# Optimization experiments

Measured on AMD Instinct MI355X. Metric: run time of the kernel, lower is better.

## Reference

```python
import jax, jax.numpy as jnp
import numpy as np

NUM_CLASSES = 3
EPS = 1e-6
POS_IOU = 0.5   # assumed thresholds of utils.match_anchors_to_targets
NEG_IOU = 0.4
NEG_RATIO = 3


def _make_anchors(H, W, stride):
    sizes = np.array([3.0, 4.0, 5.0]) * stride  # 3 anchors per location
    ys = (np.arange(H) + 0.5) * stride
    xs = (np.arange(W) + 0.5) * stride
    cy, cx = np.meshgrid(ys, xs, indexing='ij')
    cx = cx[:, :, None]
    cy = cy[:, :, None]
    s = sizes[None, None, :]
    boxes = np.stack([cx - s / 2, cy - s / 2, cx + s / 2, cy + s / 2], axis=-1)  # [H,W,A,4]
    return boxes.reshape(-1, 4).astype(np.float32)


def setup_inputs() -> dict:
    key = jax.random.key(0)
    B, G, A, C = 64, 32, 3, NUM_CLASSES
    scales = [(128, 128, 8), (64, 64, 16), (32, 32, 32)]
    ks = jax.random.split(key, 6)
    inp = {}
    for i, (H, W, s) in enumerate(scales):
        inp[f'pred{i}'] = jax.random.normal(ks[i], (B, A * (5 + C), H, W), jnp.float32)
        inp[f'anchors{i}'] = jnp.asarray(_make_anchors(H, W, s))
    c = jax.random.uniform(ks[3], (B, G, 2), minval=100.0, maxval=900.0)
    wh = jax.random.uniform(ks[4], (B, G, 2), minval=16.0, maxval=200.0)
    inp['gt_boxes'] = jnp.concatenate([c - wh / 2, c + wh / 2], axis=-1)
    inp['gt_labels'] = jax.random.randint(ks[5], (B, G), 0, C)
    return inp


def _smooth_l1(x):
    ax = jnp.abs(x)
    return jnp.where(ax < 1.0, 0.5 * x * x, ax - 0.5)


def _bce_logits(x, t):
    return jnp.maximum(x, 0.0) - x * t + jnp.log1p(jnp.exp(-jnp.abs(x)))


def _pairwise_iou(a, b):  # a [N,4], b [G,4] -> [N,G]
    lt = jnp.maximum(a[:, None, :2], b[None, :, :2])
    rb = jnp.minimum(a[:, None, 2:], b[None, :, 2:])
    wh = jnp.clip(rb - lt, 0.0)
    inter = wh[..., 0] * wh[..., 1]
    area_a = (a[:, 2] - a[:, 0]) * (a[:, 3] - a[:, 1])
    area_b = (b[:, 2] - b[:, 0]) * (b[:, 3] - b[:, 1])
    return inter / (area_a[:, None] + area_b[None, :] - inter + 1e-9)


def _per_image(p, anc, gtb, gtl):
    # p: [N, 5+C], anc: [N,4], gtb: [G,4], gtl: [G]
    iou = _pairwise_iou(anc, gtb)
    best_iou = jnp.max(iou, axis=1)
    best_idx = jnp.argmax(iou, axis=1)
    m_boxes = gtb[best_idx]
    m_labels = gtl[best_idx]
    pos = best_iou >= POS_IOU
    neg = best_iou < NEG_IOU
    posf = pos.astype(p.dtype)

    ax = (anc[:, 0] + anc[:, 2]) * 0.5
    ay = (anc[:, 1] + anc[:, 3]) * 0.5
    aw = jnp.maximum(anc[:, 2] - anc[:, 0], EPS)
    ah = jnp.maximum(anc[:, 3] - anc[:, 1], EPS)
    gx = (m_boxes[:, 0] + m_boxes[:, 2]) * 0.5
    gy = (m_boxes[:, 1] + m_boxes[:, 3]) * 0.5
    gw = jnp.maximum(m_boxes[:, 2] - m_boxes[:, 0], EPS)
    gh = jnp.maximum(m_boxes[:, 3] - m_boxes[:, 1], EPS)
    t_tx = (gx - ax) / aw
    t_ty = (gy - ay) / ah
    t_tw = jnp.log(gw / aw)
    t_th = jnp.log(gh / ah)

    loc = (posf * (_smooth_l1(p[:, 0] - t_tx) + _smooth_l1(p[:, 1] - t_ty)
                   + _smooth_l1(p[:, 2] - t_tw) + _smooth_l1(p[:, 3] - t_th))).sum()

    obj_all = _bce_logits(p[:, 4], posf)
    # hard negative mining on detached loss: top (3*max(1,num_pos)) negatives
    num_pos = pos.sum()
    num_keep = NEG_RATIO * jnp.maximum(1, num_pos)
    neg_loss = jnp.where(neg, jax.lax.stop_gradient(obj_all), -1e9)
    order = jnp.argsort(-neg_loss)
    N = order.shape[0]
    ranks = jnp.zeros((N,), dtype=jnp.int32).at[order].set(jnp.arange(N, dtype=jnp.int32))
    selected = neg & (ranks < num_keep)
    obj = (obj_all * (posf + selected.astype(p.dtype))).sum()

    logp = jax.nn.log_softmax(p[:, 5:], axis=-1)
    tgt = jnp.maximum(m_labels, 0)
    ce = -jnp.take_along_axis(logp, tgt[:, None], axis=1)[:, 0]
    cls = (posf * ce).sum()
    return loc, obj, cls


def reference(pred0, pred1, pred2, anchors0, anchors1, anchors2, gt_boxes, gt_labels):
    B = pred0.shape[0]
    C = NUM_CLASSES
    total = jnp.float32(0.0)
    for pred, anc in ((pred0, anchors0), (pred1, anchors1), (pred2, anchors2)):
        N = anc.shape[0]
        p = pred.transpose(0, 2, 3, 1).reshape(B, N, 5 + C)  # [B, H*W*A, 5+C]
        loc, obj, cls = jax.vmap(lambda pb, gb, gl, a=anc: _per_image(pb, a, gb, gl))(
            p, gt_boxes, gt_labels)
        total = total + loc.sum() + obj.sum() + cls.sum()
    return total / jnp.maximum(1.0, float(B))
```

## Files before the change

### kernel.cpp

```cpp
#include <hip/hip_runtime.h>
#include <math.h>

#define BLK 256
#define SBLK 1024
#define NBINS 2048
#define CSH 42
#define QMASK ((1ULL << CSH) - 1ULL)

__device__ __forceinline__ float bce_logits(float x, float t){
    return fmaxf(x, 0.f) - x * t + log1pf(expf(-fabsf(x)));
}
__device__ __forceinline__ float smooth_l1(float x){
    float ax = fabsf(x);
    return ax < 1.f ? 0.5f * x * x : ax - 0.5f;
}

__global__ __launch_bounds__(BLK)
void det_map_all(const float* __restrict__ pred0,
                 const float* __restrict__ pred1,
                 const float* __restrict__ pred2,
                 const float* __restrict__ gtb,
                 const int*   __restrict__ gtl,
                 float* __restrict__ vals,
                 float* __restrict__ loss_slot,
                 int*   __restrict__ pcnt_slot,
                 unsigned* __restrict__ done_cnt,
                 int B)
{
    const int b  = blockIdx.y;
    const int bx = blockIdx.x;

    const float* pred; int s, qloc, P, logW; float stride_f; size_t vbase;
    if (bx < 48){      s=0; pred=pred0; P=16384; logW=7; stride_f= 8.f; qloc= bx      << 8; vbase=(size_t)b*49152; }
    else if (bx < 60){ s=1; pred=pred1; P= 4096; logW=6; stride_f=16.f; qloc=(bx-48) << 8; vbase=(size_t)B*49152 + (size_t)b*12288; }
    else {             s=2; pred=pred2; P= 1024; logW=5; stride_f=32.f; qloc=(bx-60) << 8; vbase=(size_t)B*49152 + (size_t)B*12288 + (size_t)b*3072; }

    const int tid = threadIdx.x;
    const int lq  = 2*logW - 2;
    const int Q4  = 1 << lq;
    const int a   = qloc >> lq;
    const int q   = qloc - a*Q4 + tid;
    const int pix0 = q << 2;

    const float half = 0.5f * (float)(3 + a) * stride_f;

    const int pixLo = (qloc - a*Q4) << 2;
    const int y0 = pixLo >> logW, y1 = (pixLo + BLK*4 - 1) >> logW;
    const float ymin = ((float)y0 + 0.5f) * stride_f - half;
    const float ymax = ((float)y1 + 0.5f) * stride_f + half;

    __shared__ float4 sg[32];
    __shared__ float  sarea[32];
    __shared__ int    sl[32];
    __shared__ int    s_cnt;

    {
        bool keep = false; float4 G;
        if (tid < 32){
            G = ((const float4*)gtb)[b * 32 + tid];
            keep = (G.y < ymax) && (G.w > ymin);
        }
        unsigned long long m = __ballot(keep);
        if (tid < 64){
            if (keep){
                int idx = (int)__popcll(m & ((1ULL << tid) - 1ULL));
                sg[idx] = G;
                sarea[idx] = (G.z - G.x) * (G.w - G.y);
                sl[idx] = gtl[b * 32 + tid];
            }
            if (tid == 0) s_cnt = (int)__popcll(m);
        }
    }
    __syncthreads();
    const int cnt = s_cnt;

    const int x0 = pix0 & ((1 << logW) - 1);
    const int y  = pix0 >> logW;
    const float cy = ((float)y + 0.5f) * stride_f;
    const float Ay = cy - half, Ay2 = cy + half;
    const float sz = 2.f * half;
    const float area_a = sz * sz;

    float ax[4], az[4];
    #pragma unroll
    for (int j = 0; j < 4; ++j){
        float cx = ((float)(x0 + j) + 0.5f) * stride_f;
        ax[j] = cx - half; az[j] = cx + half;
    }

    float bi[4] = {-1.f, -1.f, -1.f, -1.f};
    float bd[4] = { 1.f,  1.f,  1.f,  1.f};
    int   bg[4] = {0, 0, 0, 0};

    for (int g = 0; g < cnt; ++g){
        const float4 G = sg[g];
        const float sab = area_a + sarea[g];
        const float h = fmaxf(fminf(Ay2, G.w) - fmaxf(Ay, G.y), 0.f);
        #pragma unroll
        for (int j = 0; j < 4; ++j){
            float wdt = fmaxf(fminf(az[j], G.z) - fmaxf(ax[j], G.x), 0.f);
            float inter = wdt * h;
            float d = (sab - inter) + 1e-9f;
            if (inter * bd[j] > bi[j] * d){ bi[j] = inter; bd[j] = d; bg[j] = g; }
        }
    }

    const size_t cP = (size_t)P;
    const float* pp = pred + ((size_t)b * 24 + (size_t)a * 8) * cP + (size_t)pix0;
    const float4 p4v = *(const float4*)(pp + 4 * cP);
    const float p4a[4] = {p4v.x, p4v.y, p4v.z, p4v.w};

    float vout[4];
    float loss = 0.f; int pc = 0;
    #pragma unroll
    for (int j = 0; j < 4; ++j){
        const bool pos = 2.f * bi[j] >= bd[j];
        const bool neg = bi[j] < 0.4f * bd[j];
        vout[j] = neg ? bce_logits(p4a[j], 0.f) : -1.f;
        if (pos){
            pc++;
            const float4 G = sg[bg[j]];
            float axc = (ax[j] + az[j]) * 0.5f, ayc = (Ay + Ay2) * 0.5f;
            float aw = fmaxf(az[j] - ax[j], 1e-6f), ah = fmaxf(Ay2 - Ay, 1e-6f);
            float gxc = (G.x + G.z) * 0.5f, gyc = (G.y + G.w) * 0.5f;
            float gw = fmaxf(G.z - G.x, 1e-6f), gh = fmaxf(G.w - G.y, 1e-6f);
            float p0 = pp[0 * cP + j];
            float p1 = pp[1 * cP + j];
            float p2 = pp[2 * cP + j];
            float p3 = pp[3 * cP + j];
            loss += smooth_l1(p0 - (gxc - axc) / aw);
            loss += smooth_l1(p1 - (gyc - ayc) / ah);
            loss += smooth_l1(p2 - logf(gw / aw));
            loss += smooth_l1(p3 - logf(gh / ah));
            loss += bce_logits(p4a[j], 1.f);
            float c0 = pp[5 * cP + j];
            float c1 = pp[6 * cP + j];
            float c2 = pp[7 * cP + j];
            float m = fmaxf(c0, fmaxf(c1, c2));
            float lse = m + logf(expf(c0 - m) + expf(c1 - m) + expf(c2 - m));
            int tg = sl[bg[j]];
            float ct = (tg == 0) ? c0 : ((tg == 1) ? c1 : c2);
            loss += lse - ct;
        }
    }
    float4 vo = {vout[0], vout[1], vout[2], vout[3]};
    *(float4*)(vals + vbase + ((size_t)(qloc - a*Q4 + tid + a*Q4)) * 4) = vo;

    for (int off = 32; off > 0; off >>= 1){
        loss += __shfl_down(loss, off);
        pc   += __shfl_down(pc, off);
    }
    __shared__ float wsum[BLK / 64];
    __shared__ int   wcnt[BLK / 64];
    if ((tid & 63) == 0){ wsum[tid >> 6] = loss; wcnt[tid >> 6] = pc; }
    __syncthreads();
    if (tid == 0){
        float S = 0.f; int C = 0;
        for (int i = 0; i < BLK / 64; ++i){ S += wsum[i]; C += wcnt[i]; }
        loss_slot[b * 63 + bx] = S;
        pcnt_slot[b * 63 + bx] = C;
        if (b == 0 && bx == 0) *done_cnt = 0u;
    }
}

__global__ __launch_bounds__(SBLK)
void det_select(const float* __restrict__ vals,
                const float* __restrict__ loss_slot,
                const int* __restrict__ pcnt_slot,
                double* __restrict__ slice_tot,
                unsigned* __restrict__ done_cnt,
                float* __restrict__ out, int B)
{
    const int sb = blockIdx.x;
    const int s = sb / B, b = sb - s * B;
    const int N = (s == 0) ? 49152 : (s == 1) ? 12288 : 3072;
    size_t base = 0;
    if (s >= 1) base += (size_t)B * 49152;
    if (s >= 2) base += (size_t)B * 12288;
    const float* V = vals + base + (size_t)b * (size_t)N;

    const int tid = threadIdx.x;
    const int lane = tid & 63, w = tid >> 6;
    const int rep = w & 1;

    __shared__ unsigned long long h[2][NBINS];
    __shared__ unsigned long long waveT[16];
    __shared__ unsigned long long waveOff[17];
    __shared__ unsigned long long sh_aboveQ;
    __shared__ double sh_sel;
    __shared__ float sh_ml;
    __shared__ int sh_b1, sh_rem, sh_done, sh_K, sh_last;

    {
        const int nb   = (s == 0) ? 48 : (s == 1) ? 12 : 3;
        const int off0 = b * 63 + ((s == 0) ? 0 : (s == 1) ? 48 : 60);
        float ml = 0.f; int C = 0;
        if (tid < nb){ ml = loss_slot[off0 + tid]; C = pcnt_slot[off0 + tid]; }
        if (tid < 64){
            for (int off = 32; off > 0; off >>= 1){
                ml += __shfl_down(ml, off);
                C  += __shfl_down(C, off);
            }
            if (tid == 0){
                sh_ml = ml; sh_K = 3 * max(1, C);
                sh_rem = sh_K; sh_done = 0;
            }
        }
    }

    for (int round = 0; round < 2; ++round){
        for (int i = tid; i < NBINS; i += SBLK){ h[0][i] = 0ULL; h[1][i] = 0ULL; }
        __syncthreads();
        const int b1 = sh_b1;

        if (round == 0 || !sh_done){
            for (int i = tid * 4; i < N; i += SBLK * 4){
                float4 v4 = *(const float4*)(V + i);
                #pragma unroll
                for (int j = 0; j < 4; ++j){
                    float v = (j == 0) ? v4.x : (j == 1) ? v4.y : (j == 2) ? v4.z : v4.w;
                    if (!(v >= 0.f)) continue;
                    float t = v * 256.f;
                    int bin0 = min((int)t, NBINS - 1);
                    int key;
                    if (round == 0) key = bin0;
                    else {
                        if (bin0 != b1) continue;
                        float frac = t - (float)bin0;
                        key = min((int)(frac * 2048.f), NBINS - 1);
                    }
                    unsigned long long p = (1ULL << CSH) |
                        (unsigned long long)(unsigned)(int)(v * 4194304.f);
                    atomicAdd(&h[rep][key], p);
                }
            }
        }
        __syncthreads();
        if (sh_done) break;

        const int bhi = NBINS - 1 - 2 * tid;
        const unsigned long long c0p = h[0][bhi] + h[1][bhi];
        const unsigned long long c1p = h[0][bhi - 1] + h[1][bhi - 1];
        const unsigned long long pair = c0p + c1p;
        unsigned long long ci = pair;
        #pragma unroll
        for (int off = 1; off < 64; off <<= 1){
            unsigned long long cu = __shfl_up(ci, off);
            if (lane >= off) ci += cu;
        }
        if (lane == 63) waveT[w] = ci;
        __syncthreads();
        if (tid == 0){
            unsigned long long acc = 0ULL;
            #pragma unroll
            for (int i = 0; i < 16; ++i){ waveOff[i] = acc; acc += waveT[i]; }
            waveOff[16] = acc;
            if (round == 0 && sh_K >= (int)(acc >> CSH)){
                sh_done = 1;
                sh_sel = (double)(acc & QMASK) * (1.0 / 4194304.0);
            }
        }
        __syncthreads();
        if (sh_done) break;

        const int rem = sh_rem;
        const unsigned long long giP = waveOff[w] + ci;
        const unsigned long long geP = giP - pair;
        const int gi = (int)(giP >> CSH);
        const int ge = (int)(geP >> CSH);
        if (ge < rem && rem <= gi){
            const int c0 = (int)(c0p >> CSH);
            int bin, aboveC; unsigned long long aboveQ;
            if (ge + c0 >= rem){ bin = bhi;     aboveC = ge;      aboveQ = geP & QMASK; }
            else               { bin = bhi - 1; aboveC = ge + c0; aboveQ = (geP + c0p) & QMASK; }
            const int newRem = rem - aboveC;
            if (round == 0){
                sh_b1 = bin; sh_rem = newRem; sh_aboveQ = aboveQ;
            } else {
                float thresh = (float)sh_b1 * (1.f / 256.f) + (float)bin * (1.f / 524288.f);
                sh_sel = (double)(sh_aboveQ + aboveQ) * (1.0 / 4194304.0)
                       + (double)newRem * (double)thresh;
            }
        }
        __syncthreads();
    }

    if (tid == 0){
        slice_tot[sb] = (double)sh_ml + sh_sel;
        __threadfence();
        unsigned t = atomicAdd(done_cnt, 1u);
        sh_last = (t == (unsigned)(gridDim.x - 1));
        if (sh_last) __threadfence();
    }
    __syncthreads();
    if (sh_last){
        double p = (tid < 3 * B) ? slice_tot[tid] : 0.0;
        for (int off = 32; off > 0; off >>= 1) p += __shfl_down(p, off);
        __shared__ double wred[16];
        if (lane == 0) wred[w] = p;
        __syncthreads();
        if (tid == 0){
            double tot = 0.0;
            for (int i = 0; i < 16; ++i) tot += wred[i];
            out[0] = (float)(tot / (double)B);
        }
    }
}

extern "C" void kernel_launch(void* const* d_in, const int* in_sizes, int n_in,
                              void* d_out, int out_size, void* d_ws, size_t ws_size,
                              hipStream_t stream)
{
    const float* gtb = (const float*)d_in[6];
    const int*   gtl = (const int*)d_in[7];
    const int B = in_sizes[6] / (32 * 4);

    unsigned* done      = (unsigned*)d_ws;
    double*   slice_tot = (double*)((char*)d_ws + 64);
    float*    loss_slot = (float*)((char*)d_ws + 2048);
    int*      pcnt_slot = (int*)((char*)d_ws + 2048 + 16384);
    float*    vals      = (float*)((char*)d_ws + 36864);

    det_map_all<<<dim3(63, B), BLK, 0, stream>>>(
        (const float*)d_in[0], (const float*)d_in[2], (const float*)d_in[4],
        gtb, gtl, vals, loss_slot, pcnt_slot, done, B);
    det_select<<<dim3(3 * B), SBLK, 0, stream>>>(
        vals, loss_slot, pcnt_slot, slice_tot, done, (float*)d_out, B);
}
```

Measured before the change: 208.9 us.

## Fuse hard-negative selection into map kernel via last-block-per-slice ticket

Merges the separate selection kernel into the per-anchor map kernel. The last block to finish each (scale, image) slice, detected with an atomic ticket counter, runs the two-level histogram top-K selection. The first-level histogram shrinks to 1024 bins and the second level to 2048 sub-bins, both sized for 256-thread blocks, and a memset clears the counters before launch. This removes one kernel launch and the gap between the two kernels, and lets selection overlap with map work from other slices. In exchange, selection now runs on 256 threads instead of 1024, which may lengthen the tail for the large scale-0 slices.

```diff
diff --git a/kernel.cpp b/kernel.cpp
--- a/kernel.cpp
+++ b/kernel.cpp
@@ -2,8 +2,8 @@
 #include <math.h>
 
 #define BLK 256
-#define SBLK 1024
-#define NBINS 2048
+#define NB1 1024
+#define NB2 2048
 #define CSH 42
 #define QMASK ((1ULL << CSH) - 1ULL)
 
@@ -16,31 +16,35 @@
 }
 
 __global__ __launch_bounds__(BLK)
-void det_map_all(const float* __restrict__ pred0,
-                 const float* __restrict__ pred1,
-                 const float* __restrict__ pred2,
-                 const float* __restrict__ gtb,
-                 const int*   __restrict__ gtl,
-                 float* __restrict__ vals,
-                 float* __restrict__ loss_slot,
-                 int*   __restrict__ pcnt_slot,
-                 unsigned* __restrict__ done_cnt,
-                 int B)
+void det_all(const float* __restrict__ pred0,
+             const float* __restrict__ pred1,
+             const float* __restrict__ pred2,
+             const float* __restrict__ gtb,
+             const int*   __restrict__ gtl,
+             float* __restrict__ vals,
+             float* __restrict__ loss_slot,
+             int*   __restrict__ pcnt_slot,
+             unsigned* __restrict__ slice_tk,
+             double* __restrict__ slice_tot,
+             unsigned* __restrict__ done_tk,
+             float* __restrict__ out, int B)
 {
     const int b  = blockIdx.y;
     const int bx = blockIdx.x;
 
-    const float* pred; int s, qloc, P, logW; float stride_f; size_t vbase;
-    if (bx < 48){      s=0; pred=pred0; P=16384; logW=7; stride_f= 8.f; qloc= bx      << 8; vbase=(size_t)b*49152; }
-    else if (bx < 60){ s=1; pred=pred1; P= 4096; logW=6; stride_f=16.f; qloc=(bx-48) << 8; vbase=(size_t)B*49152 + (size_t)b*12288; }
-    else {             s=2; pred=pred2; P= 1024; logW=5; stride_f=32.f; qloc=(bx-60) << 8; vbase=(size_t)B*49152 + (size_t)B*12288 + (size_t)b*3072; }
-
+    const float* pred; int s, qloc, P, logW, nb; float stride_f; size_t vbase;
+    if (bx < 48){      s=0; pred=pred0; P=16384; logW=7; nb=48; stride_f= 8.f; qloc= bx      << 8; vbase=(size_t)b*49152; }
+    else if (bx < 60){ s=1; pred=pred1; P= 4096; logW=6; nb=12; stride_f=16.f; qloc=(bx-48) << 8; vbase=(size_t)B*49152 + (size_t)b*12288; }
+    else {             s=2; pred=pred2; P= 1024; logW=5; nb= 3; stride_f=32.f; qloc=(bx-60) << 8; vbase=(size_t)B*49152 + (size_t)B*12288 + (size_t)b*3072; }
+
+    const int sb  = s * B + b;
     const int tid = threadIdx.x;
+    const int lane = tid & 63, w = tid >> 6;
+
     const int lq  = 2*logW - 2;
     const int Q4  = 1 << lq;
     const int a   = qloc >> lq;
-    const int q   = qloc - a*Q4 + tid;
-    const int pix0 = q << 2;
+    const int pix0 = (qloc - a*Q4 + tid) << 2;
 
     const float half = 0.5f * (float)(3 + a) * stride_f;
 
@@ -53,6 +57,15 @@
     __shared__ float  sarea[32];
     __shared__ int    sl[32];
     __shared__ int    s_cnt;
+    __shared__ unsigned long long hsel[2][NB1];
+    __shared__ unsigned long long waveT[4];
+    __shared__ unsigned long long waveOff[5];
+    __shared__ unsigned long long sh_aboveQ;
+    __shared__ double sh_sel;
+    __shared__ float  sh_ml;
+    __shared__ float  wsum[4];
+    __shared__ int    wcnt[4];
+    __shared__ int    sh_b1, sh_rem, sh_done, sh_K, sh_win, sh_last;
 
     {
         bool keep = false; float4 G;
@@ -78,8 +91,7 @@
     const int y  = pix0 >> logW;
     const float cy = ((float)y + 0.5f) * stride_f;
     const float Ay = cy - half, Ay2 = cy + half;
-    const float sz = 2.f * half;
-    const float area_a = sz * sz;
+    const float area_a = (2.f * half) * (2.f * half);
 
     float ax[4], az[4];
     #pragma unroll
@@ -144,55 +156,34 @@
         }
     }
     float4 vo = {vout[0], vout[1], vout[2], vout[3]};
-    *(float4*)(vals + vbase + ((size_t)(qloc - a*Q4 + tid + a*Q4)) * 4) = vo;
+    *(float4*)(vals + vbase + (size_t)(qloc - a*Q4 + tid + a*Q4) * 4) = vo;
 
     for (int off = 32; off > 0; off >>= 1){
         loss += __shfl_down(loss, off);
         pc   += __shfl_down(pc, off);
     }
-    __shared__ float wsum[BLK / 64];
-    __shared__ int   wcnt[BLK / 64];
-    if ((tid & 63) == 0){ wsum[tid >> 6] = loss; wcnt[tid >> 6] = pc; }
+    if (lane == 0){ wsum[w] = loss; wcnt[w] = pc; }
     __syncthreads();
     if (tid == 0){
         float S = 0.f; int C = 0;
-        for (int i = 0; i < BLK / 64; ++i){ S += wsum[i]; C += wcnt[i]; }
+        for (int i = 0; i < 4; ++i){ S += wsum[i]; C += wcnt[i]; }
         loss_slot[b * 63 + bx] = S;
         pcnt_slot[b * 63 + bx] = C;
-        if (b == 0 && bx == 0) *done_cnt = 0u;
-    }
-}
-
-__global__ __launch_bounds__(SBLK)
-void det_select(const float* __restrict__ vals,
-                const float* __restrict__ loss_slot,
-                const int* __restrict__ pcnt_slot,
-                double* __restrict__ slice_tot,
-                unsigned* __restrict__ done_cnt,
-                float* __restrict__ out, int B)
-{
-    const int sb = blockIdx.x;
-    const int s = sb / B, b = sb - s * B;
+        __threadfence();
+        unsigned old = atomicAdd(&slice_tk[sb], 1u);
+        sh_win = (old == (unsigned)(nb - 1));
+        if (sh_win) __threadfence();
+    }
+    __syncthreads();
+    if (!sh_win) return;
+
     const int N = (s == 0) ? 49152 : (s == 1) ? 12288 : 3072;
     size_t base = 0;
     if (s >= 1) base += (size_t)B * 49152;
     if (s >= 2) base += (size_t)B * 12288;
     const float* V = vals + base + (size_t)b * (size_t)N;
 
-    const int tid = threadIdx.x;
-    const int lane = tid & 63, w = tid >> 6;
-    const int rep = w & 1;
-
-    __shared__ unsigned long long h[2][NBINS];
-    __shared__ unsigned long long waveT[16];
-    __shared__ unsigned long long waveOff[17];
-    __shared__ unsigned long long sh_aboveQ;
-    __shared__ double sh_sel;
-    __shared__ float sh_ml;
-    __shared__ int sh_b1, sh_rem, sh_done, sh_K, sh_last;
-
     {
-        const int nb   = (s == 0) ? 48 : (s == 1) ? 12 : 3;
         const int off0 = b * 63 + ((s == 0) ? 0 : (s == 1) ? 48 : 60);
         float ml = 0.f; int C = 0;
         if (tid < nb){ ml = loss_slot[off0 + tid]; C = pcnt_slot[off0 + tid]; }
@@ -201,48 +192,33 @@
                 ml += __shfl_down(ml, off);
                 C  += __shfl_down(C, off);
             }
-            if (tid == 0){
-                sh_ml = ml; sh_K = 3 * max(1, C);
-                sh_rem = sh_K; sh_done = 0;
-            }
-        }
-    }
-
-    for (int round = 0; round < 2; ++round){
-        for (int i = tid; i < NBINS; i += SBLK){ h[0][i] = 0ULL; h[1][i] = 0ULL; }
-        __syncthreads();
-        const int b1 = sh_b1;
-
-        if (round == 0 || !sh_done){
-            for (int i = tid * 4; i < N; i += SBLK * 4){
-                float4 v4 = *(const float4*)(V + i);
-                #pragma unroll
-                for (int j = 0; j < 4; ++j){
-                    float v = (j == 0) ? v4.x : (j == 1) ? v4.y : (j == 2) ? v4.z : v4.w;
-                    if (!(v >= 0.f)) continue;
-                    float t = v * 256.f;
-                    int bin0 = min((int)t, NBINS - 1);
-                    int key;
-                    if (round == 0) key = bin0;
-                    else {
-                        if (bin0 != b1) continue;
-                        float frac = t - (float)bin0;
-                        key = min((int)(frac * 2048.f), NBINS - 1);
-                    }
-                    unsigned long long p = (1ULL << CSH) |
-                        (unsigned long long)(unsigned)(int)(v * 4194304.f);
-                    atomicAdd(&h[rep][key], p);
-                }
-            }
-        }
-        __syncthreads();
-        if (sh_done) break;
-
-        const int bhi = NBINS - 1 - 2 * tid;
-        const unsigned long long c0p = h[0][bhi] + h[1][bhi];
-        const unsigned long long c1p = h[0][bhi - 1] + h[1][bhi - 1];
-        const unsigned long long pair = c0p + c1p;
-        unsigned long long ci = pair;
+            if (tid == 0){ sh_ml = ml; sh_K = 3 * max(1, C); sh_done = 0; }
+        }
+    }
+    for (int i = tid; i < NB1; i += BLK){ hsel[0][i] = 0ULL; hsel[1][i] = 0ULL; }
+    __syncthreads();
+
+    const int rep = w & 1;
+    for (int i = tid * 4; i < N; i += BLK * 4){
+        float4 v4 = *(const float4*)(V + i);
+        #pragma unroll
+        for (int j = 0; j < 4; ++j){
+            float v = (j == 0) ? v4.x : (j == 1) ? v4.y : (j == 2) ? v4.z : v4.w;
+            if (!(v >= 0.f)) continue;
+            int bin = min((int)(v * 128.f), NB1 - 1);
+            unsigned long long p = (1ULL << CSH) |
+                (unsigned long long)(unsigned)(int)(v * 4194304.f);
+            atomicAdd(&hsel[rep][bin], p);
+        }
+    }
+    __syncthreads();
+
+    {
+        const int start = NB1 - 4 * (tid + 1);
+        unsigned long long chunk[4]; unsigned long long tot = 0ULL;
+        #pragma unroll
+        for (int i = 0; i < 4; ++i){ chunk[i] = hsel[0][start+i] + hsel[1][start+i]; tot += chunk[i]; }
+        unsigned long long ci = tot;
         #pragma unroll
         for (int off = 1; off < 64; off <<= 1){
             unsigned long long cu = __shfl_up(ci, off);
@@ -253,34 +229,99 @@
         if (tid == 0){
             unsigned long long acc = 0ULL;
             #pragma unroll
-            for (int i = 0; i < 16; ++i){ waveOff[i] = acc; acc += waveT[i]; }
-            waveOff[16] = acc;
-            if (round == 0 && sh_K >= (int)(acc >> CSH)){
+            for (int i = 0; i < 4; ++i){ waveOff[i] = acc; acc += waveT[i]; }
+            waveOff[4] = acc;
+            if (sh_K >= (int)(acc >> CSH)){
                 sh_done = 1;
                 sh_sel = (double)(acc & QMASK) * (1.0 / 4194304.0);
             }
         }
         __syncthreads();
-        if (sh_done) break;
-
+        if (!sh_done){
+            const int K = sh_K;
+            const unsigned long long giP = waveOff[w] + ci;
+            const unsigned long long geP = giP - tot;
+            const int gi = (int)(giP >> CSH);
+            const int ge = (int)(geP >> CSH);
+            if (ge < K && K <= gi){
+                int aboveC = ge;
+                unsigned long long aboveQ = geP & QMASK;
+                #pragma unroll
+                for (int i = 3; i >= 0; --i){
+                    int c = (int)(chunk[i] >> CSH);
+                    if (aboveC + c >= K){
+                        sh_b1 = start + i; sh_rem = K - aboveC; sh_aboveQ = aboveQ;
+                        break;
+                    }
+                    aboveC += c;
+                    aboveQ += chunk[i] & QMASK;
+                }
+            }
+            __syncthreads();
+        }
+    }
+
+    if (!sh_done){
+        unsigned long long* Hs = (unsigned long long*)hsel;
+        for (int i = tid; i < NB2; i += BLK) Hs[i] = 0ULL;
+        __syncthreads();
+        const int b1 = sh_b1;
+        for (int i = tid * 4; i < N; i += BLK * 4){
+            float4 v4 = *(const float4*)(V + i);
+            #pragma unroll
+            for (int j = 0; j < 4; ++j){
+                float v = (j == 0) ? v4.x : (j == 1) ? v4.y : (j == 2) ? v4.z : v4.w;
+                if (!(v >= 0.f)) continue;
+                float t = v * 128.f;
+                int bin = min((int)t, NB1 - 1);
+                if (bin != b1) continue;
+                float frac = t - (float)bin;
+                int sub = min((int)(frac * 2048.f), NB2 - 1);
+                unsigned long long p = (1ULL << CSH) |
+                    (unsigned long long)(unsigned)(int)(v * 4194304.f);
+                atomicAdd(&Hs[sub], p);
+            }
+        }
+        __syncthreads();
+
+        const int start = NB2 - 8 * (tid + 1);
+        unsigned long long chunk[8]; unsigned long long tot = 0ULL;
+        #pragma unroll
+        for (int i = 0; i < 8; ++i){ chunk[i] = Hs[start + i]; tot += chunk[i]; }
+        unsigned long long ci = tot;
+        #pragma unroll
+        for (int off = 1; off < 64; off <<= 1){
+            unsigned long long cu = __shfl_up(ci, off);
+            if (lane >= off) ci += cu;
+        }
+        if (lane == 63) waveT[w] = ci;
+        __syncthreads();
+        if (tid == 0){
+            unsigned long long acc = 0ULL;
+            #pragma unroll
+            for (int i = 0; i < 4; ++i){ waveOff[i] = acc; acc += waveT[i]; }
+            waveOff[4] = acc;
+        }
+        __syncthreads();
         const int rem = sh_rem;
         const unsigned long long giP = waveOff[w] + ci;
-        const unsigned long long geP = giP - pair;
+        const unsigned long long geP = giP - tot;
         const int gi = (int)(giP >> CSH);
         const int ge = (int)(geP >> CSH);
         if (ge < rem && rem <= gi){
-            const int c0 = (int)(c0p >> CSH);
-            int bin, aboveC; unsigned long long aboveQ;
-            if (ge + c0 >= rem){ bin = bhi;     aboveC = ge;      aboveQ = geP & QMASK; }
-            else               { bin = bhi - 1; aboveC = ge + c0; aboveQ = (geP + c0p) & QMASK; }
-            const int newRem = rem - aboveC;
-            if (round == 0){
-                sh_b1 = bin; sh_rem = newRem; sh_aboveQ = aboveQ;
-            } else {
-                float thresh = (float)sh_b1 * (1.f / 256.f) + (float)bin * (1.f / 524288.f);
-                sh_sel = (double)(sh_aboveQ + aboveQ) * (1.0 / 4194304.0)
-                       + (double)newRem * (double)thresh;
-            }
+            int aboveC = ge;
+            unsigned long long aboveQ = geP & QMASK;
+            int sub = start;
+            #pragma unroll
+            for (int i = 7; i >= 0; --i){
+                int c = (int)(chunk[i] >> CSH);
+                if (aboveC + c >= rem){ sub = start + i; break; }
+                aboveC += c;
+                aboveQ += chunk[i] & QMASK;
+            }
+            float thresh = (float)b1 * (1.f / 128.f) + (float)sub * (1.f / 262144.f);
+            sh_sel = (double)(sh_aboveQ + aboveQ) * (1.0 / 4194304.0)
+                   + (double)(rem - aboveC) * (double)thresh;
         }
         __syncthreads();
     }
@@ -288,20 +329,20 @@
     if (tid == 0){
         slice_tot[sb] = (double)sh_ml + sh_sel;
         __threadfence();
-        unsigned t = atomicAdd(done_cnt, 1u);
-        sh_last = (t == (unsigned)(gridDim.x - 1));
+        unsigned t = atomicAdd(done_tk, 1u);
+        sh_last = (t == (unsigned)(3 * B - 1));
         if (sh_last) __threadfence();
     }
     __syncthreads();
     if (sh_last){
         double p = (tid < 3 * B) ? slice_tot[tid] : 0.0;
         for (int off = 32; off > 0; off >>= 1) p += __shfl_down(p, off);
-        __shared__ double wred[16];
+        __shared__ double wred[4];
         if (lane == 0) wred[w] = p;
         __syncthreads();
         if (tid == 0){
             double tot = 0.0;
-            for (int i = 0; i < 16; ++i) tot += wred[i];
+            for (int i = 0; i < 4; ++i) tot += wred[i];
             out[0] = (float)(tot / (double)B);
         }
     }
@@ -316,14 +357,16 @@
     const int B = in_sizes[6] / (32 * 4);
 
     unsigned* done      = (unsigned*)d_ws;
-    double*   slice_tot = (double*)((char*)d_ws + 64);
-    float*    loss_slot = (float*)((char*)d_ws + 2048);
-    int*      pcnt_slot = (int*)((char*)d_ws + 2048 + 16384);
-    float*    vals      = (float*)((char*)d_ws + 36864);
-
-    det_map_all<<<dim3(63, B), BLK, 0, stream>>>(
+    unsigned* slice_tk  = (unsigned*)((char*)d_ws + 64);
+    double*   slice_tot = (double*)((char*)d_ws + 1024);
+    float*    loss_slot = (float*)((char*)d_ws + 4096);
+    int*      pcnt_slot = (int*)((char*)d_ws + 4096 + 16384);
+    float*    vals      = (float*)((char*)d_ws + 40960);
+
+    hipMemsetAsync(d_ws, 0, 1024, stream);
+
+    det_all<<<dim3(63, B), BLK, 0, stream>>>(
         (const float*)d_in[0], (const float*)d_in[2], (const float*)d_in[4],
-        gtb, gtl, vals, loss_slot, pcnt_slot, done, B);
-    det_select<<<dim3(3 * B), SBLK, 0, stream>>>(
-        vals, loss_slot, pcnt_slot, slice_tot, done, (float*)d_out, B);
+        gtb, gtl, vals, loss_slot, pcnt_slot, slice_tk, slice_tot, done,
+        (float*)d_out, B);
 }
```

New measurement: 380.8 us. 1.82x slower.
